# Optimization experiments

Measured on AMD Instinct MI355X. Metric: run time of the kernel, lower is better.

The kernel has to match this reference:

```python
import jax, jax.numpy as jnp
import numpy as np

N = 4096
CIN = 128
COUT = 128
J = 2
SLOPE = 0.2        # LeakyReLU negative slope (GAT-style)
NEG = -9.0e15      # mask fill value from the source
ATT = J * COUT     # att_slice


def _leaky(v):
    return jnp.where(v >= 0, v, SLOPE * v)


def setup_inputs() -> dict:
    key = jax.random.key(0)
    ks = jax.random.split(key, 12)
    x = jax.random.normal(ks[0], (N, CIN), dtype=jnp.float32)

    def sparse_op(k):
        kv, km = jax.random.split(k)
        vals = jax.random.normal(kv, (N, N), dtype=jnp.float32)
        mask = jax.random.uniform(km, (N, N)) < 0.05
        return jnp.where(mask, vals, 0.0)

    Lu = sparse_op(ks[1])
    Ld = sparse_op(ks[2])
    P = jax.random.normal(ks[3], (N, N), dtype=jnp.float32) * 0.01  # harmonic projector

    s = 1.0 / np.sqrt(CIN)
    Wi_w = jax.random.uniform(ks[4], (J, CIN, COUT), minval=-s, maxval=s)
    Wi_b = jax.random.uniform(ks[5], (J, COUT), minval=-s, maxval=s)
    Ws_w = jax.random.uniform(ks[6], (J, CIN, COUT), minval=-s, maxval=s)
    Ws_b = jax.random.uniform(ks[7], (J, COUT), minval=-s, maxval=s)
    Wh_w = jax.random.uniform(ks[8], (CIN, COUT), minval=-s, maxval=s)
    Wh_b = jax.random.uniform(ks[9], (COUT,), minval=-s, maxval=s)
    att_irr = jax.random.normal(ks[10], (2 * ATT, 1), dtype=jnp.float32) * 0.1
    att_sol = jax.random.normal(ks[11], (2 * ATT, 1), dtype=jnp.float32) * 0.1
    return {"x": x, "Lu": Lu, "Ld": Ld, "P": P,
            "Wi_w": Wi_w, "Wi_b": Wi_b, "Ws_w": Ws_w, "Ws_b": Ws_b,
            "Wh_w": Wh_w, "Wh_b": Wh_b, "att_irr": att_irr, "att_sol": att_sol}


def reference(x, Lu, Ld, P, Wi_w, Wi_b, Ws_w, Ws_b, Wh_w, Wh_b, att_irr, att_sol):
    n = x.shape[0]
    # concat_j W_irr[j](x) -> [N, J*COUT] (j-major matches torch.cat along dim=1)
    x_irr = (jnp.einsum('nc,jco->njo', x, Wi_w) + Wi_b[None]).reshape(n, ATT)
    x_sol = (jnp.einsum('nc,jco->njo', x, Ws_w) + Ws_b[None]).reshape(n, ATT)

    # GAT-style scores: E[i,j] = leaky(s1[i] + s2[j])
    E_irr = _leaky(x_irr @ att_irr[:ATT] + (x_irr @ att_irr[ATT:]).T)
    E_sol = _leaky(x_sol @ att_sol[:ATT] + (x_sol @ att_sol[ATT:]).T)
    E_irr = jnp.where(Ld != 0, E_irr, NEG)
    E_sol = jnp.where(Lu != 0, E_sol, NEG)
    alpha_irr = jax.nn.softmax(E_irr, axis=1)  # dropout: eval mode -> identity
    alpha_sol = jax.nn.softmax(E_sol, axis=1)

    z = (alpha_irr @ x) @ Wi_w[0] + Wi_b[0] + (alpha_sol @ x) @ Ws_w[0] + Ws_b[0]
    for p in range(1, J):  # Laplacian-power aggregation
        alpha_irr = alpha_irr @ Ld
        alpha_sol = alpha_sol @ Lu
        z = z + (alpha_irr @ x) @ Wi_w[p] + Wi_b[p]
        z = z + (alpha_sol @ x) @ Ws_w[p] + Ws_b[p]
    z = z + (P @ x) @ Wh_w + Wh_b
    return z
```

## Files before the change

kernel.cpp:

```cpp
#include <hip/hip_runtime.h>

#define NN 4096
#define IDX_CAP 512
#define SLOPE 0.2f

typedef float f4_t __attribute__((ext_vector_type(4)));
typedef __bf16 bf8v __attribute__((ext_vector_type(8)));
typedef float f32x16 __attribute__((ext_vector_type(16)));

#define V_OFF     0
#define C_OFF     512
#define BT_OFF    516
#define S_OFF     1024
#define HXI_OFF   32768
#define HXS_OFF   (HXI_OFF + NN*128)
#define UI_OFF    (HXS_OFF + NN*128)
#define US_OFF    (UI_OFF + NN*128)
#define XWH_OFF   (US_OFF + NN*128)
#define OI_OFF    (XWH_OFF + NN*128)
#define OS_OFF    (OI_OFF + NN*128)
#define ZP_OFF    (OS_OFF + NN*128)
#define WS_FLOATS (ZP_OFF + 8*NN*128)
#define IDX_BYTE_OFF ((size_t)WS_FLOATS * 4)
#define CNT_BYTE_OFF (IDX_BYTE_OFF + (size_t)2*NN*IDX_CAP*2)

#define XI(c)   ((c) + (((c) >> 5) << 2))

#define BMAP_BR(bid)    (((bid) >> 2) & 1)
#define BMAP_RBLK(bid)  ((((bid) >> 3) << 2) | ((bid) & 3))

#define FRAG(c, k) ((size_t)((k) >> 4) * 2048 + (size_t)((c) >> 5) * 512 \
                    + (size_t)((((c) & 31) + 32 * (((k) >> 3) & 1)) * 8 + ((k) & 7)))

__device__ __forceinline__ unsigned short f2bf(float x) {
  unsigned u = __float_as_uint(x);
  return (unsigned short)((u + 0x7FFFu + ((u >> 16) & 1u)) >> 16);
}
__device__ __forceinline__ float bf2f(unsigned short h) {
  return __uint_as_float(((unsigned)h) << 16);
}
union BFU { unsigned short u[8]; bf8v v; };

__global__ __launch_bounds__(128) void k_prep(
    const float* __restrict__ Wi_w, const float* __restrict__ Wi_b,
    const float* __restrict__ Ws_w, const float* __restrict__ Ws_b,
    const float* __restrict__ Wh_b, const float* __restrict__ att_irr,
    const float* __restrict__ att_sol, float* __restrict__ ws) {
  const int t = threadIdx.x;
  float v1i = 0.f, v2i = 0.f, v1s = 0.f, v2s = 0.f;
  for (int j = 0; j < 2; ++j) {
    for (int o = 0; o < 128; ++o) {
      const float wi = Wi_w[j*16384 + t*128 + o];
      const float wv = Ws_w[j*16384 + t*128 + o];
      v1i += wi * att_irr[j*128 + o];
      v2i += wi * att_irr[256 + j*128 + o];
      v1s += wv * att_sol[j*128 + o];
      v2s += wv * att_sol[256 + j*128 + o];
    }
  }
  ws[V_OFF + t]       = v1i;
  ws[V_OFF + 128 + t] = v2i;
  ws[V_OFF + 256 + t] = v1s;
  ws[V_OFF + 384 + t] = v2s;
  ws[BT_OFF + t] = Wi_b[t] + Wi_b[128 + t] + Ws_b[t] + Ws_b[128 + t] + Wh_b[t];
  if (t < 4) {
    const float* bb = (t < 2) ? Wi_b : Ws_b;
    const float* aa = ((t < 2) ? att_irr : att_sol) + ((t & 1) ? 256 : 0);
    float c = 0.f;
    for (int k = 0; k < 256; ++k) c += bb[k] * aa[k];
    ws[C_OFF + t] = c;
  }
}

__global__ __launch_bounds__(256) void k_pre2(
    const float* __restrict__ x, const float* __restrict__ Wh_w,
    float* __restrict__ ws, unsigned short* __restrict__ xth,
    unsigned short* __restrict__ xtl) {
  __shared__ __align__(16) float At[32][33];
  __shared__ __align__(16) float Wt[32][144];
  const int t = threadIdx.x;

  if (blockIdx.x < 128) {
    const int rb = blockIdx.x;
    const int rg = t >> 4, cg = t & 15;
    const int r0 = rb * 32;
    float acc[2][8];
    #pragma unroll
    for (int i = 0; i < 2; ++i)
      #pragma unroll
      for (int j = 0; j < 8; ++j) acc[i][j] = 0.f;
    for (int k0 = 0; k0 < 128; k0 += 32) {
      __syncthreads();
      {
        const int row = t >> 3, kq = t & 7;
        const float4 av = *(const float4*)&x[(r0 + row)*128 + k0 + kq*4];
        At[row][kq*4+0] = av.x; At[row][kq*4+1] = av.y;
        At[row][kq*4+2] = av.z; At[row][kq*4+3] = av.w;
      }
      #pragma unroll
      for (int l = 0; l < 4; ++l) {
        const int idx = t + l*256;
        const int kr = idx >> 5, c4 = idx & 31;
        const float4 wv = *(const float4*)&Wh_w[(k0 + kr)*128 + c4*4];
        *(float4*)&Wt[kr][XI(c4*4)] = wv;
      }
      __syncthreads();
      #pragma unroll
      for (int k = 0; k < 32; ++k) {
        const float a0 = At[rg*2 + 0][k];
        const float a1 = At[rg*2 + 1][k];
        const float4 b0 = *(const float4*)&Wt[k][XI(cg*8)];
        const float4 b1 = *(const float4*)&Wt[k][XI(cg*8 + 4)];
        acc[0][0] += a0*b0.x; acc[0][1] += a0*b0.y; acc[0][2] += a0*b0.z; acc[0][3] += a0*b0.w;
        acc[0][4] += a0*b1.x; acc[0][5] += a0*b1.y; acc[0][6] += a0*b1.z; acc[0][7] += a0*b1.w;
        acc[1][0] += a1*b0.x; acc[1][1] += a1*b0.y; acc[1][2] += a1*b0.z; acc[1][3] += a1*b0.w;
        acc[1][4] += a1*b1.x; acc[1][5] += a1*b1.y; acc[1][6] += a1*b1.z; acc[1][7] += a1*b1.w;
      }
    }
    #pragma unroll
    for (int i = 0; i < 2; ++i) {
      const int r = r0 + rg*2 + i;
      #pragma unroll
      for (int j = 0; j < 8; ++j) {
        const int c = cg*8 + j;
        const float val = acc[i][j];
        const unsigned short h = f2bf(val);
        const unsigned short l = f2bf(val - bf2f(h));
        const size_t fa = FRAG(c, r);
        xth[fa] = h;
        xtl[fa] = l;
      }
    }
  } else {
    const int wave = t >> 6, lane = t & 63;
    const int row = (blockIdx.x - 128) * 4 + wave;
    const float* v = ws + V_OFF;
    const float x0 = x[row*128 + lane];
    const float x1 = x[row*128 + 64 + lane];
    float p0 = x0 * v[lane]       + x1 * v[64 + lane];
    float p1 = x0 * v[128 + lane] + x1 * v[192 + lane];
    float p2 = x0 * v[256 + lane] + x1 * v[320 + lane];
    float p3 = x0 * v[384 + lane] + x1 * v[448 + lane];
    #pragma unroll
    for (int off = 32; off; off >>= 1) {
      p0 += __shfl_down(p0, off);
      p1 += __shfl_down(p1, off);
      p2 += __shfl_down(p2, off);
      p3 += __shfl_down(p3, off);
    }
    if (lane == 0) {
      ws[S_OFF + row]          = p0 + ws[C_OFF + 0];
      ws[S_OFF + NN + row]     = p1 + ws[C_OFF + 1];
      ws[S_OFF + 2*NN + row]   = p2 + ws[C_OFF + 2];
      ws[S_OFF + 3*NN + row]   = p3 + ws[C_OFF + 3];
    }
  }
}

__global__ __launch_bounds__(256) void k_spmm_emit(
    const float* __restrict__ Ld, const float* __restrict__ Lu,
    const float* __restrict__ x, float* __restrict__ ws,
    unsigned short* __restrict__ idxbuf, int* __restrict__ cntbuf) {
  const int bid = blockIdx.x;
  const int br  = BMAP_BR(bid);
  const int w = threadIdx.x >> 6, lane = threadIdx.x & 63;
  const int row = BMAP_RBLK(bid) * 4 + w;
  const float* __restrict__ Lrow = (br ? Lu : Ld) + (size_t)row * NN;
  float* __restrict__ Hx = ws + (br ? HXS_OFF : HXI_OFF);
  unsigned short* __restrict__ idxg = idxbuf + (size_t)(br*NN + row) * IDX_CAP;
  const unsigned long long lmask = (1ull << lane) - 1ull;

  __shared__ short jl[4][IDX_CAP];
  __shared__ float vl[4][IDX_CAP];

  const f4_t* __restrict__ Lrow4 = (const f4_t*)Lrow;
  int base = 0;
  #pragma unroll
  for (int c = 0; c < 4; ++c) {
    f4_t lv[4];
    #pragma unroll
    for (int i = 0; i < 4; ++i)
      lv[i] = __builtin_nontemporal_load(&Lrow4[c*256 + i*64 + lane]);
    #pragma unroll
    for (int i = 0; i < 4; ++i) {
      #pragma unroll
      for (int cc = 0; cc < 4; ++cc) {
        const float v = lv[i][cc];
        const unsigned long long bm = __ballot(v != 0.f);
        if (v != 0.f) {
          const int pos = base + (int)__popcll(bm & lmask);
          if (pos < IDX_CAP) {
            jl[w][pos] = (short)((c*256 + i*64 + lane)*4 + cc);
            vl[w][pos] = v;
          }
        }
        base += (int)__popcll(bm);
      }
    }
  }
  const int m = base;
  if (lane == 0) cntbuf[br*NN + row] = m;

  if (m <= IDX_CAP) {
    for (int p = lane; p < m; p += 64) idxg[p] = (unsigned short)jl[w][p];

    const f4_t* __restrict__ x4 = (const f4_t*)x;
    const int li = lane & 31, half = lane >> 5;
    f4_t acc = {0.f, 0.f, 0.f, 0.f};
    int p = 0;
    for (; 2*(p + 3) + 1 < m; p += 4) {
      int jj[4]; float vv[4];
      #pragma unroll
      for (int u = 0; u < 4; ++u) {
        const int q = 2*(p + u) + half;
        jj[u] = jl[w][q]; vv[u] = vl[w][q];
      }
      f4_t gg[4];
      #pragma unroll
      for (int u = 0; u < 4; ++u) gg[u] = x4[jj[u]*32 + li];
      #pragma unroll
      for (int u = 0; u < 4; ++u) acc += vv[u] * gg[u];
    }
    for (; 2*p < m; ++p) {
      const int q = 2*p + half;
      if (q < m) acc += vl[w][q] * x4[jl[w][q]*32 + li];
    }
    #pragma unroll
    for (int c = 0; c < 4; ++c) acc[c] += __shfl_xor(acc[c], 32);
    if (half == 0) *(f4_t*)&Hx[row*128 + li*4] = acc;
  } else {
    const float2* __restrict__ x2 = (const float2*)x;
    float acc0 = 0.f, acc1 = 0.f;
    for (int j = 0; j < NN; ++j) {
      const float v = Lrow[j];
      if (v != 0.f) {
        const float2 g = x2[j*64 + lane];
        acc0 += v*g.x; acc1 += v*g.y;
      }
    }
    Hx[row*128 + lane*2]     = acc0;
    Hx[row*128 + lane*2 + 1] = acc1;
  }
}

__global__ __launch_bounds__(256) void k_ugemm(
    const float* __restrict__ x, const float* __restrict__ Wi_w,
    const float* __restrict__ Ws_w, float* __restrict__ ws) {
  const int rb = blockIdx.x;
  const int sel = blockIdx.y;
  const float* A[2]; const float* W[2]; float* out;
  if (sel == 0) { A[0]=x; W[0]=Wi_w; A[1]=ws+HXI_OFF; W[1]=Wi_w+16384; out=ws+UI_OFF; }
  else          { A[0]=x; W[0]=Ws_w; A[1]=ws+HXS_OFF; W[1]=Ws_w+16384; out=ws+US_OFF; }

  __shared__ __align__(16) float At[32][33];
  __shared__ __align__(16) float Wt[32][144];
  const int t = threadIdx.x;
  const int rg = t >> 4, cg = t & 15;
  const int r0 = rb * 32;
  float acc[2][8];
  #pragma unroll
  for (int i = 0; i < 2; ++i)
    #pragma unroll
    for (int j = 0; j < 8; ++j) acc[i][j] = 0.f;

  for (int ps = 0; ps < 2; ++ps) {
    const float* __restrict__ Ap = A[ps];
    const float* __restrict__ Wp = W[ps];
    for (int k0 = 0; k0 < 128; k0 += 32) {
      __syncthreads();
      {
        const int row = t >> 3, kq = t & 7;
        const float4 av = *(const float4*)&Ap[(r0 + row)*128 + k0 + kq*4];
        At[row][kq*4+0] = av.x; At[row][kq*4+1] = av.y;
        At[row][kq*4+2] = av.z; At[row][kq*4+3] = av.w;
      }
      #pragma unroll
      for (int l = 0; l < 4; ++l) {
        const int idx = t + l*256;
        const int kr = idx >> 5, c4 = idx & 31;
        const float4 wv = *(const float4*)&Wp[(k0 + kr)*128 + c4*4];
        *(float4*)&Wt[kr][XI(c4*4)] = wv;
      }
      __syncthreads();
      #pragma unroll
      for (int k = 0; k < 32; ++k) {
        const float a0 = At[rg*2 + 0][k];
        const float a1 = At[rg*2 + 1][k];
        const float4 b0 = *(const float4*)&Wt[k][XI(cg*8)];
        const float4 b1 = *(const float4*)&Wt[k][XI(cg*8 + 4)];
        acc[0][0] += a0*b0.x; acc[0][1] += a0*b0.y; acc[0][2] += a0*b0.z; acc[0][3] += a0*b0.w;
        acc[0][4] += a0*b1.x; acc[0][5] += a0*b1.y; acc[0][6] += a0*b1.z; acc[0][7] += a0*b1.w;
        acc[1][0] += a1*b0.x; acc[1][1] += a1*b0.y; acc[1][2] += a1*b0.z; acc[1][3] += a1*b0.w;
        acc[1][4] += a1*b1.x; acc[1][5] += a1*b1.y; acc[1][6] += a1*b1.z; acc[1][7] += a1*b1.w;
      }
    }
  }
  #pragma unroll
  for (int i = 0; i < 2; ++i) {
    const int r = r0 + rg*2 + i;
    #pragma unroll
    for (int j = 0; j < 8; ++j) out[r*128 + cg*8 + j] = acc[i][j];
  }
}

__global__ __launch_bounds__(256) void k_attn(
    const float* __restrict__ Ld, const float* __restrict__ Lu,
    float* __restrict__ ws, const unsigned short* __restrict__ idxbuf,
    const int* __restrict__ cntbuf) {
  const int bid = blockIdx.x;
  const int br  = BMAP_BR(bid);
  const int w = threadIdx.x >> 6, lane = threadIdx.x & 63;
  const int row = BMAP_RBLK(bid) * 4 + w;
  const float* __restrict__ U = ws + (br ? US_OFF : UI_OFF);
  float* __restrict__ O = ws + (br ? OS_OFF : OI_OFF);
  const float s1 = ws[S_OFF + (br ? 2*NN : 0) + row];
  const float* __restrict__ s2a = ws + S_OFF + (br ? 3*NN : NN);
  const int cnt = cntbuf[br*NN + row];

  __shared__ short jl[4][IDX_CAP];
  __shared__ float el[4][IDX_CAP];

  if (cnt > 0 && cnt <= IDX_CAP) {
    const unsigned short* __restrict__ idx = idxbuf + (size_t)(br*NN + row) * IDX_CAP;
    float dpart = 0.f;
    for (int p = lane; p < cnt; p += 64) {
      const int j = idx[p];
      const float sc = s1 + s2a[j];
      const float e = expf(sc >= 0.f ? sc : SLOPE * sc);
      jl[w][p] = (short)j; el[w][p] = e; dpart += e;
    }
    #pragma unroll
    for (int off = 32; off; off >>= 1) dpart += __shfl_xor(dpart, off);
    const float rden = 1.f / dpart;

    const f4_t* __restrict__ U4 = (const f4_t*)U;
    const int li = lane & 31, half = lane >> 5;
    f4_t acc = {0.f, 0.f, 0.f, 0.f};
    int p = 0;
    for (; 2*(p + 3) + 1 < cnt; p += 4) {
      int jj[4]; float ee[4];
      #pragma unroll
      for (int u = 0; u < 4; ++u) {
        const int q = 2*(p + u) + half;
        jj[u] = jl[w][q]; ee[u] = el[w][q];
      }
      f4_t gg[4];
      #pragma unroll
      for (int u = 0; u < 4; ++u) gg[u] = U4[jj[u]*32 + li];
      #pragma unroll
      for (int u = 0; u < 4; ++u) acc += ee[u] * gg[u];
    }
    for (; 2*p < cnt; ++p) {
      const int q = 2*p + half;
      if (q < cnt) acc += el[w][q] * U4[jl[w][q]*32 + li];
    }
    #pragma unroll
    for (int c = 0; c < 4; ++c) acc[c] += __shfl_xor(acc[c], 32);
    if (half == 0) {
      acc *= rden;
      *(f4_t*)&O[row*128 + li*4] = acc;
    }
  } else if (cnt == 0) {
    const float2* __restrict__ U2 = (const float2*)U;
    float acc0 = 0.f, acc1 = 0.f;
    for (int j = 0; j < NN; ++j) {
      const float2 g = U2[j*64 + lane];
      acc0 += g.x; acc1 += g.y;
    }
    O[row*128 + lane*2]     = acc0 * (1.f / NN);
    O[row*128 + lane*2 + 1] = acc1 * (1.f / NN);
  } else {
    const float* __restrict__ Lrow = (br ? Lu : Ld) + (size_t)row * NN;
    const float2* __restrict__ U2 = (const float2*)U;
    float acc0 = 0.f, acc1 = 0.f, dp = 0.f;
    for (int j = 0; j < NN; ++j) {
      const float v = Lrow[j];
      if (v != 0.f) {
        const float sc = s1 + s2a[j];
        const float e = expf(sc >= 0.f ? sc : SLOPE * sc);
        const float2 g = U2[j*64 + lane];
        acc0 += e*g.x; acc1 += e*g.y;
        dp += e;
      }
    }
    O[row*128 + lane*2]     = acc0 / dp;
    O[row*128 + lane*2 + 1] = acc1 / dp;
  }
}

__global__ __launch_bounds__(256) void k_pgemm(
    const float* __restrict__ P, const unsigned short* __restrict__ xth,
    const unsigned short* __restrict__ xtl, float* __restrict__ zpart) {
  const int t = threadIdx.x;
  const int w = t >> 6, lane = t & 63;
  const int la = lane & 31;
  const int koff = (lane >> 5) * 8;
  const int r0 = blockIdx.x * 32;
  const int kz = blockIdx.y;
  const int kb = kz * 512 + w * 128;

  f32x16 acc[4];
  #pragma unroll
  for (int n = 0; n < 4; ++n)
    #pragma unroll
    for (int e = 0; e < 16; ++e) acc[n][e] = 0.f;

  const float* __restrict__ arow = P + (size_t)(r0 + la) * NN + kb + koff;
  const unsigned short* __restrict__ bh_base = xth + (size_t)kb * 128 + lane * 8;
  const unsigned short* __restrict__ bl_base = xtl + (size_t)kb * 128 + lane * 8;

  f4_t a0 = __builtin_nontemporal_load((const f4_t*)arow);
  f4_t a1 = __builtin_nontemporal_load((const f4_t*)(arow + 4));
  for (int s = 0; s < 8; ++s) {
    f4_t na0 = a0, na1 = a1;
    if (s < 7) {
      na0 = __builtin_nontemporal_load((const f4_t*)(arow + (s + 1) * 16));
      na1 = __builtin_nontemporal_load((const f4_t*)(arow + (s + 1) * 16 + 4));
    }
    BFU ah, al;
    #pragma unroll
    for (int i = 0; i < 8; ++i) {
      const float f = (i < 4) ? a0[i] : a1[i - 4];
      const unsigned short h = f2bf(f);
      ah.u[i] = h;
      al.u[i] = f2bf(f - bf2f(h));
    }
    const unsigned short* __restrict__ bh_s = bh_base + s * 2048;
    const unsigned short* __restrict__ bl_s = bl_base + s * 2048;
    #pragma unroll
    for (int n = 0; n < 4; ++n) {
      const bf8v bh = *(const bf8v*)(bh_s + n * 512);
      const bf8v bl = *(const bf8v*)(bl_s + n * 512);
      acc[n] = __builtin_amdgcn_mfma_f32_32x32x16_bf16(ah.v, bh, acc[n], 0, 0, 0);
      acc[n] = __builtin_amdgcn_mfma_f32_32x32x16_bf16(al.v, bh, acc[n], 0, 0, 0);
      acc[n] = __builtin_amdgcn_mfma_f32_32x32x16_bf16(ah.v, bl, acc[n], 0, 0, 0);
    }
    a0 = na0; a1 = na1;
  }

  __shared__ float red[2][32][128];
  if (w < 2) {
    #pragma unroll
    for (int n = 0; n < 4; ++n)
      #pragma unroll
      for (int reg = 0; reg < 16; ++reg) {
        const int row = (reg & 3) + 8*(reg >> 2) + 4*(lane >> 5);
        red[w][row][32*n + la] = acc[n][reg];
      }
  }
  __syncthreads();
  if (w >= 2) {
    #pragma unroll
    for (int n = 0; n < 4; ++n)
      #pragma unroll
      for (int reg = 0; reg < 16; ++reg) {
        const int row = (reg & 3) + 8*(reg >> 2) + 4*(lane >> 5);
        red[w - 2][row][32*n + la] += acc[n][reg];
      }
  }
  __syncthreads();
  float* __restrict__ zp = zpart + (size_t)kz * NN * 128;
  #pragma unroll
  for (int i = 0; i < 8; ++i) {
    const int row = w * 8 + i;
    zp[(size_t)(r0 + row) * 128 + lane]      = red[0][row][lane]      + red[1][row][lane];
    zp[(size_t)(r0 + row) * 128 + 64 + lane] = red[0][row][64 + lane] + red[1][row][64 + lane];
  }
}

__global__ __launch_bounds__(256) void k_combine(const float* __restrict__ ws,
                                                 float* __restrict__ z) {
  const int i = blockIdx.x * 256 + threadIdx.x;
  const int col = i & 127;
  float acc = ws[BT_OFF + col] + ws[OI_OFF + i] + ws[OS_OFF + i];
  #pragma unroll
  for (int kz = 0; kz < 8; ++kz) acc += ws[ZP_OFF + kz*NN*128 + i];
  z[i] = acc;
}

extern "C" void kernel_launch(void* const* d_in, const int* in_sizes, int n_in,
                              void* d_out, int out_size, void* d_ws, size_t ws_size,
                              hipStream_t stream) {
  const float* x       = (const float*)d_in[0];
  const float* Lu      = (const float*)d_in[1];
  const float* Ld      = (const float*)d_in[2];
  const float* P       = (const float*)d_in[3];
  const float* Wi_w    = (const float*)d_in[4];
  const float* Wi_b    = (const float*)d_in[5];
  const float* Ws_w    = (const float*)d_in[6];
  const float* Ws_b    = (const float*)d_in[7];
  const float* Wh_w    = (const float*)d_in[8];
  const float* Wh_b    = (const float*)d_in[9];
  const float* att_irr = (const float*)d_in[10];
  const float* att_sol = (const float*)d_in[11];
  float* z  = (float*)d_out;
  float* ws = (float*)d_ws;
  unsigned short* idxbuf = (unsigned short*)((char*)d_ws + IDX_BYTE_OFF);
  int*            cntbuf = (int*)((char*)d_ws + CNT_BYTE_OFF);
  float*          zpart  = ws + ZP_OFF;
  unsigned short* xth    = (unsigned short*)(ws + XWH_OFF);
  unsigned short* xtl    = xth + (size_t)128 * NN;

  k_prep<<<1, 128, 0, stream>>>(Wi_w, Wi_b, Ws_w, Ws_b, Wh_b, att_irr, att_sol, ws);
  k_pre2<<<1152, 256, 0, stream>>>(x, Wh_w, ws, xth, xtl);
  k_spmm_emit<<<2 * NN / 4, 256, 0, stream>>>(Ld, Lu, x, ws, idxbuf, cntbuf);
  {
    dim3 g(128, 2);
    k_ugemm<<<g, 256, 0, stream>>>(x, Wi_w, Ws_w, ws);
  }
  k_attn<<<2 * NN / 4, 256, 0, stream>>>(Ld, Lu, ws, idxbuf, cntbuf);
  {
    dim3 g(128, 8);
    k_pgemm<<<g, 256, 0, stream>>>(P, xth, xtl, zpart);
  }
  k_combine<<<NN * 128 / 256, 256, 0, stream>>>(ws, z);
}
```

Baseline: 354.7 us.

## Replace sparse gather SpMM and attention with dense split-bf16 MFMA GEMMs

The per-row nonzero compaction plus gather-based SpMM for L·x, and the index-based attention aggregation, are replaced by dense MFMA GEMMs over the full 4096-wide rows. Values are split into hi and lo bf16 parts and combined with three MFMAs to keep near-fp32 accuracy. The attention kernel computes masked exp scores inline and reduces the denominator across the 8 waves. This drops the index buffers and the divergent gathers, but does dense work on 5%-sparse matrices and launches only 256 blocks. The softmax max-subtraction is still omitted, and the empty-row fallback is gone, so a row with no nonzeros now divides by zero.

Result: slower. 444.3 us (+25.3%).

```diff
diff --git a/kernel.cpp b/kernel.cpp
--- a/kernel.cpp
+++ b/kernel.cpp
@@ -22,7 +22,6 @@
 #define ZP_OFF    (OS_OFF + NN*128)
 #define WS_FLOATS (ZP_OFF + 8*NN*128)
 #define IDX_BYTE_OFF ((size_t)WS_FLOATS * 4)
-#define CNT_BYTE_OFF (IDX_BYTE_OFF + (size_t)2*NN*IDX_CAP*2)
 
 #define XI(c)   ((c) + (((c) >> 5) << 2))
 
@@ -75,7 +74,8 @@
 __global__ __launch_bounds__(256) void k_pre2(
     const float* __restrict__ x, const float* __restrict__ Wh_w,
     float* __restrict__ ws, unsigned short* __restrict__ xth,
-    unsigned short* __restrict__ xtl) {
+    unsigned short* __restrict__ xtl, unsigned short* __restrict__ xfh,
+    unsigned short* __restrict__ xfl) {
   __shared__ __align__(16) float At[32][33];
   __shared__ __align__(16) float Wt[32][144];
   const int t = threadIdx.x;
@@ -137,6 +137,16 @@
     const float* v = ws + V_OFF;
     const float x0 = x[row*128 + lane];
     const float x1 = x[row*128 + 64 + lane];
+    {
+      const unsigned short h0 = f2bf(x0);
+      const unsigned short l0 = f2bf(x0 - bf2f(h0));
+      const size_t fa0 = FRAG(lane, row);
+      xfh[fa0] = h0; xfl[fa0] = l0;
+      const unsigned short h1 = f2bf(x1);
+      const unsigned short l1 = f2bf(x1 - bf2f(h1));
+      const size_t fa1 = FRAG(lane + 64, row);
+      xfh[fa1] = h1; xfl[fa1] = l1;
+    }
     float p0 = x0 * v[lane]       + x1 * v[64 + lane];
     float p1 = x0 * v[128 + lane] + x1 * v[192 + lane];
     float p2 = x0 * v[256 + lane] + x1 * v[320 + lane];
@@ -157,100 +167,105 @@
   }
 }
 
-__global__ __launch_bounds__(256) void k_spmm_emit(
+__global__ __launch_bounds__(512) void k_hxmm(
     const float* __restrict__ Ld, const float* __restrict__ Lu,
-    const float* __restrict__ x, float* __restrict__ ws,
-    unsigned short* __restrict__ idxbuf, int* __restrict__ cntbuf) {
+    const unsigned short* __restrict__ xfh, const unsigned short* __restrict__ xfl,
+    float* __restrict__ ws) {
   const int bid = blockIdx.x;
   const int br  = BMAP_BR(bid);
-  const int w = threadIdx.x >> 6, lane = threadIdx.x & 63;
-  const int row = BMAP_RBLK(bid) * 4 + w;
-  const float* __restrict__ Lrow = (br ? Lu : Ld) + (size_t)row * NN;
+  const int rblk = BMAP_RBLK(bid);
+  const int t = threadIdx.x;
+  const int w = t >> 6, lane = t & 63;
+  const int la = lane & 31;
+  const int koff = (lane >> 5) * 8;
+  const int r0 = rblk * 32;
+  const int kb = w * 512;
+  const float* __restrict__ L = br ? Lu : Ld;
   float* __restrict__ Hx = ws + (br ? HXS_OFF : HXI_OFF);
-  unsigned short* __restrict__ idxg = idxbuf + (size_t)(br*NN + row) * IDX_CAP;
-  const unsigned long long lmask = (1ull << lane) - 1ull;
-
-  __shared__ short jl[4][IDX_CAP];
-  __shared__ float vl[4][IDX_CAP];
-
-  const f4_t* __restrict__ Lrow4 = (const f4_t*)Lrow;
-  int base = 0;
-  #pragma unroll
-  for (int c = 0; c < 4; ++c) {
-    f4_t lv[4];
-    #pragma unroll
-    for (int i = 0; i < 4; ++i)
-      lv[i] = __builtin_nontemporal_load(&Lrow4[c*256 + i*64 + lane]);
-    #pragma unroll
-    for (int i = 0; i < 4; ++i) {
-      #pragma unroll
-      for (int cc = 0; cc < 4; ++cc) {
-        const float v = lv[i][cc];
-        const unsigned long long bm = __ballot(v != 0.f);
-        if (v != 0.f) {
-          const int pos = base + (int)__popcll(bm & lmask);
-          if (pos < IDX_CAP) {
-            jl[w][pos] = (short)((c*256 + i*64 + lane)*4 + cc);
-            vl[w][pos] = v;
-          }
-        }
-        base += (int)__popcll(bm);
-      }
-    }
-  }
-  const int m = base;
-  if (lane == 0) cntbuf[br*NN + row] = m;
-
-  if (m <= IDX_CAP) {
-    for (int p = lane; p < m; p += 64) idxg[p] = (unsigned short)jl[w][p];
-
-    const f4_t* __restrict__ x4 = (const f4_t*)x;
-    const int li = lane & 31, half = lane >> 5;
-    f4_t acc = {0.f, 0.f, 0.f, 0.f};
-    int p = 0;
-    for (; 2*(p + 3) + 1 < m; p += 4) {
-      int jj[4]; float vv[4];
-      #pragma unroll
-      for (int u = 0; u < 4; ++u) {
-        const int q = 2*(p + u) + half;
-        jj[u] = jl[w][q]; vv[u] = vl[w][q];
-      }
-      f4_t gg[4];
-      #pragma unroll
-      for (int u = 0; u < 4; ++u) gg[u] = x4[jj[u]*32 + li];
-      #pragma unroll
-      for (int u = 0; u < 4; ++u) acc += vv[u] * gg[u];
-    }
-    for (; 2*p < m; ++p) {
-      const int q = 2*p + half;
-      if (q < m) acc += vl[w][q] * x4[jl[w][q]*32 + li];
-    }
-    #pragma unroll
-    for (int c = 0; c < 4; ++c) acc[c] += __shfl_xor(acc[c], 32);
-    if (half == 0) *(f4_t*)&Hx[row*128 + li*4] = acc;
-  } else {
-    const float2* __restrict__ x2 = (const float2*)x;
-    float acc0 = 0.f, acc1 = 0.f;
-    for (int j = 0; j < NN; ++j) {
-      const float v = Lrow[j];
-      if (v != 0.f) {
-        const float2 g = x2[j*64 + lane];
-        acc0 += v*g.x; acc1 += v*g.y;
-      }
-    }
-    Hx[row*128 + lane*2]     = acc0;
-    Hx[row*128 + lane*2 + 1] = acc1;
+
+  f32x16 acc[4];
+  #pragma unroll
+  for (int n = 0; n < 4; ++n)
+    #pragma unroll
+    for (int e = 0; e < 16; ++e) acc[n][e] = 0.f;
+
+  const float* __restrict__ arow = L + (size_t)(r0 + la) * NN + kb + koff;
+  const unsigned short* __restrict__ bh_base = xfh + (size_t)kb * 128 + lane * 8;
+  const unsigned short* __restrict__ bl_base = xfl + (size_t)kb * 128 + lane * 8;
+
+  f4_t a0 = __builtin_nontemporal_load((const f4_t*)arow);
+  f4_t a1 = __builtin_nontemporal_load((const f4_t*)(arow + 4));
+  for (int s = 0; s < 32; ++s) {
+    f4_t na0 = a0, na1 = a1;
+    if (s < 31) {
+      na0 = __builtin_nontemporal_load((const f4_t*)(arow + (s + 1) * 16));
+      na1 = __builtin_nontemporal_load((const f4_t*)(arow + (s + 1) * 16 + 4));
+    }
+    BFU ah, al;
+    #pragma unroll
+    for (int i = 0; i < 8; ++i) {
+      const float f = (i < 4) ? a0[i] : a1[i - 4];
+      const unsigned short h = f2bf(f);
+      ah.u[i] = h;
+      al.u[i] = f2bf(f - bf2f(h));
+    }
+    const unsigned short* __restrict__ bh_s = bh_base + s * 2048;
+    const unsigned short* __restrict__ bl_s = bl_base + s * 2048;
+    #pragma unroll
+    for (int n = 0; n < 4; ++n) {
+      const bf8v bh = *(const bf8v*)(bh_s + n * 512);
+      const bf8v bl = *(const bf8v*)(bl_s + n * 512);
+      acc[n] = __builtin_amdgcn_mfma_f32_32x32x16_bf16(ah.v, bh, acc[n], 0, 0, 0);
+      acc[n] = __builtin_amdgcn_mfma_f32_32x32x16_bf16(al.v, bh, acc[n], 0, 0, 0);
+      acc[n] = __builtin_amdgcn_mfma_f32_32x32x16_bf16(ah.v, bl, acc[n], 0, 0, 0);
+    }
+    a0 = na0; a1 = na1;
+  }
+
+  __shared__ float red[4][32][128];
+  if (w < 4) {
+    #pragma unroll
+    for (int n = 0; n < 4; ++n)
+      #pragma unroll
+      for (int reg = 0; reg < 16; ++reg) {
+        const int row = (reg & 3) + 8*(reg >> 2) + 4*(lane >> 5);
+        red[w][row][32*n + la] = acc[n][reg];
+      }
+  }
+  __syncthreads();
+  if (w >= 4) {
+    #pragma unroll
+    for (int n = 0; n < 4; ++n)
+      #pragma unroll
+      for (int reg = 0; reg < 16; ++reg) {
+        const int row = (reg & 3) + 8*(reg >> 2) + 4*(lane >> 5);
+        red[w - 4][row][32*n + la] += acc[n][reg];
+      }
+  }
+  __syncthreads();
+  {
+    const int row = t >> 4;
+    const int c0 = (t & 15) * 8;
+    #pragma unroll
+    for (int j = 0; j < 8; ++j) {
+      const int c = c0 + j;
+      Hx[(size_t)(r0 + row) * 128 + c] =
+          red[0][row][c] + red[1][row][c] + red[2][row][c] + red[3][row][c];
+    }
   }
 }
 
 __global__ __launch_bounds__(256) void k_ugemm(
     const float* __restrict__ x, const float* __restrict__ Wi_w,
-    const float* __restrict__ Ws_w, float* __restrict__ ws) {
+    const float* __restrict__ Ws_w, float* __restrict__ ws,
+    unsigned short* __restrict__ uih, unsigned short* __restrict__ uil,
+    unsigned short* __restrict__ ush, unsigned short* __restrict__ usl) {
   const int rb = blockIdx.x;
   const int sel = blockIdx.y;
-  const float* A[2]; const float* W[2]; float* out;
-  if (sel == 0) { A[0]=x; W[0]=Wi_w; A[1]=ws+HXI_OFF; W[1]=Wi_w+16384; out=ws+UI_OFF; }
-  else          { A[0]=x; W[0]=Ws_w; A[1]=ws+HXS_OFF; W[1]=Ws_w+16384; out=ws+US_OFF; }
+  const float* A[2]; const float* W[2];
+  unsigned short* uh; unsigned short* ul;
+  if (sel == 0) { A[0]=x; W[0]=Wi_w; A[1]=ws+HXI_OFF; W[1]=Wi_w+16384; uh=uih; ul=uil; }
+  else          { A[0]=x; W[0]=Ws_w; A[1]=ws+HXS_OFF; W[1]=Ws_w+16384; uh=ush; ul=usl; }
 
   __shared__ __align__(16) float At[32][33];
   __shared__ __align__(16) float Wt[32][144];
@@ -299,92 +314,121 @@
   for (int i = 0; i < 2; ++i) {
     const int r = r0 + rg*2 + i;
     #pragma unroll
-    for (int j = 0; j < 8; ++j) out[r*128 + cg*8 + j] = acc[i][j];
-  }
-}
-
-__global__ __launch_bounds__(256) void k_attn(
+    for (int j = 0; j < 8; ++j) {
+      const int c = cg*8 + j;
+      const float val = acc[i][j];
+      const unsigned short h = f2bf(val);
+      const unsigned short l = f2bf(val - bf2f(h));
+      const size_t fa = FRAG(c, r);
+      uh[fa] = h;
+      ul[fa] = l;
+    }
+  }
+}
+
+__global__ __launch_bounds__(512) void k_attnmm(
     const float* __restrict__ Ld, const float* __restrict__ Lu,
-    float* __restrict__ ws, const unsigned short* __restrict__ idxbuf,
-    const int* __restrict__ cntbuf) {
+    float* __restrict__ ws, const unsigned short* __restrict__ uih,
+    const unsigned short* __restrict__ uil, const unsigned short* __restrict__ ush,
+    const unsigned short* __restrict__ usl) {
   const int bid = blockIdx.x;
   const int br  = BMAP_BR(bid);
-  const int w = threadIdx.x >> 6, lane = threadIdx.x & 63;
-  const int row = BMAP_RBLK(bid) * 4 + w;
-  const float* __restrict__ U = ws + (br ? US_OFF : UI_OFF);
+  const int rblk = BMAP_RBLK(bid);
+  const int t = threadIdx.x;
+  const int w = t >> 6, lane = t & 63;
+  const int la = lane & 31;
+  const int koff = (lane >> 5) * 8;
+  const int r0 = rblk * 32;
+  const int kb = w * 512;
+  const float* __restrict__ L = br ? Lu : Ld;
+  const unsigned short* __restrict__ ufh = br ? ush : uih;
+  const unsigned short* __restrict__ ufl = br ? usl : uil;
   float* __restrict__ O = ws + (br ? OS_OFF : OI_OFF);
-  const float s1 = ws[S_OFF + (br ? 2*NN : 0) + row];
-  const float* __restrict__ s2a = ws + S_OFF + (br ? 3*NN : NN);
-  const int cnt = cntbuf[br*NN + row];
-
-  __shared__ short jl[4][IDX_CAP];
-  __shared__ float el[4][IDX_CAP];
-
-  if (cnt > 0 && cnt <= IDX_CAP) {
-    const unsigned short* __restrict__ idx = idxbuf + (size_t)(br*NN + row) * IDX_CAP;
-    float dpart = 0.f;
-    for (int p = lane; p < cnt; p += 64) {
-      const int j = idx[p];
-      const float sc = s1 + s2a[j];
-      const float e = expf(sc >= 0.f ? sc : SLOPE * sc);
-      jl[w][p] = (short)j; el[w][p] = e; dpart += e;
-    }
-    #pragma unroll
-    for (int off = 32; off; off >>= 1) dpart += __shfl_xor(dpart, off);
-    const float rden = 1.f / dpart;
-
-    const f4_t* __restrict__ U4 = (const f4_t*)U;
-    const int li = lane & 31, half = lane >> 5;
-    f4_t acc = {0.f, 0.f, 0.f, 0.f};
-    int p = 0;
-    for (; 2*(p + 3) + 1 < cnt; p += 4) {
-      int jj[4]; float ee[4];
-      #pragma unroll
-      for (int u = 0; u < 4; ++u) {
-        const int q = 2*(p + u) + half;
-        jj[u] = jl[w][q]; ee[u] = el[w][q];
-      }
-      f4_t gg[4];
-      #pragma unroll
-      for (int u = 0; u < 4; ++u) gg[u] = U4[jj[u]*32 + li];
-      #pragma unroll
-      for (int u = 0; u < 4; ++u) acc += ee[u] * gg[u];
-    }
-    for (; 2*p < cnt; ++p) {
-      const int q = 2*p + half;
-      if (q < cnt) acc += el[w][q] * U4[jl[w][q]*32 + li];
-    }
-    #pragma unroll
-    for (int c = 0; c < 4; ++c) acc[c] += __shfl_xor(acc[c], 32);
-    if (half == 0) {
-      acc *= rden;
-      *(f4_t*)&O[row*128 + li*4] = acc;
-    }
-  } else if (cnt == 0) {
-    const float2* __restrict__ U2 = (const float2*)U;
-    float acc0 = 0.f, acc1 = 0.f;
-    for (int j = 0; j < NN; ++j) {
-      const float2 g = U2[j*64 + lane];
-      acc0 += g.x; acc1 += g.y;
-    }
-    O[row*128 + lane*2]     = acc0 * (1.f / NN);
-    O[row*128 + lane*2 + 1] = acc1 * (1.f / NN);
-  } else {
-    const float* __restrict__ Lrow = (br ? Lu : Ld) + (size_t)row * NN;
-    const float2* __restrict__ U2 = (const float2*)U;
-    float acc0 = 0.f, acc1 = 0.f, dp = 0.f;
-    for (int j = 0; j < NN; ++j) {
-      const float v = Lrow[j];
-      if (v != 0.f) {
-        const float sc = s1 + s2a[j];
-        const float e = expf(sc >= 0.f ? sc : SLOPE * sc);
-        const float2 g = U2[j*64 + lane];
-        acc0 += e*g.x; acc1 += e*g.y;
-        dp += e;
-      }
-    }
-    O[row*128 + lane*2]     = acc0 / dp;
-    O[row*128 + lane*2 + 1] = acc1 / dp;
+  const float s1v = ws[S_OFF + (br ? 2*NN : 0) + r0 + la];
+  const float* __restrict__ s2p = ws + S_OFF + (br ? 3*NN : NN) + kb + koff;
+
+  f32x16 acc[4];
+  #pragma unroll
+  for (int n = 0; n < 4; ++n)
+    #pragma unroll
+    for (int e = 0; e < 16; ++e) acc[n][e] = 0.f;
+  float dp = 0.f;
+
+  const float* __restrict__ arow = L + (size_t)(r0 + la) * NN + kb + koff;
+  const unsigned short* __restrict__ bh_base = ufh + (size_t)kb * 128 + lane * 8;
+  const unsigned short* __restrict__ bl_base = ufl + (size_t)kb * 128 + lane * 8;
+
+  f4_t a0 = __builtin_nontemporal_load((const f4_t*)arow);
+  f4_t a1 = __builtin_nontemporal_load((const f4_t*)(arow + 4));
+  for (int s = 0; s < 32; ++s) {
+    f4_t na0 = a0, na1 = a1;
+    if (s < 31) {
+      na0 = __builtin_nontemporal_load((const f4_t*)(arow + (s + 1) * 16));
+      na1 = __builtin_nontemporal_load((const f4_t*)(arow + (s + 1) * 16 + 4));
+    }
+    const f4_t s2a = *(const f4_t*)(s2p + s * 16);
+    const f4_t s2b = *(const f4_t*)(s2p + s * 16 + 4);
+    BFU eh, el;
+    #pragma unroll
+    for (int i = 0; i < 8; ++i) {
+      const float Lv = (i < 4) ? a0[i] : a1[i - 4];
+      const float s2 = (i < 4) ? s2a[i] : s2b[i - 4];
+      const float sc = s1v + s2;
+      const float ex = (Lv != 0.f) ? expf(sc >= 0.f ? sc : SLOPE * sc) : 0.f;
+      dp += ex;
+      const unsigned short h = f2bf(ex);
+      eh.u[i] = h;
+      el.u[i] = f2bf(ex - bf2f(h));
+    }
+    const unsigned short* __restrict__ bh_s = bh_base + s * 2048;
+    const unsigned short* __restrict__ bl_s = bl_base + s * 2048;
+    #pragma unroll
+    for (int n = 0; n < 4; ++n) {
+      const bf8v bh = *(const bf8v*)(bh_s + n * 512);
+      const bf8v bl = *(const bf8v*)(bl_s + n * 512);
+      acc[n] = __builtin_amdgcn_mfma_f32_32x32x16_bf16(eh.v, bh, acc[n], 0, 0, 0);
+      acc[n] = __builtin_amdgcn_mfma_f32_32x32x16_bf16(el.v, bh, acc[n], 0, 0, 0);
+      acc[n] = __builtin_amdgcn_mfma_f32_32x32x16_bf16(eh.v, bl, acc[n], 0, 0, 0);
+    }
+    a0 = na0; a1 = na1;
+  }
+  dp += __shfl_xor(dp, 32);
+
+  __shared__ float red[4][32][128];
+  __shared__ float dsl[4][32];
+  if (w < 4) {
+    #pragma unroll
+    for (int n = 0; n < 4; ++n)
+      #pragma unroll
+      for (int reg = 0; reg < 16; ++reg) {
+        const int row = (reg & 3) + 8*(reg >> 2) + 4*(lane >> 5);
+        red[w][row][32*n + la] = acc[n][reg];
+      }
+    if (lane < 32) dsl[w][la] = dp;
+  }
+  __syncthreads();
+  if (w >= 4) {
+    #pragma unroll
+    for (int n = 0; n < 4; ++n)
+      #pragma unroll
+      for (int reg = 0; reg < 16; ++reg) {
+        const int row = (reg & 3) + 8*(reg >> 2) + 4*(lane >> 5);
+        red[w - 4][row][32*n + la] += acc[n][reg];
+      }
+    if (lane < 32) dsl[w - 4][la] += dp;
+  }
+  __syncthreads();
+  {
+    const int row = t >> 4;
+    const int c0 = (t & 15) * 8;
+    const float den = dsl[0][row] + dsl[1][row] + dsl[2][row] + dsl[3][row];
+    const float rden = 1.f / den;
+    #pragma unroll
+    for (int j = 0; j < 8; ++j) {
+      const int c = c0 + j;
+      O[(size_t)(r0 + row) * 128 + c] =
+          (red[0][row][c] + red[1][row][c] + red[2][row][c] + red[3][row][c]) * rden;
+    }
   }
 }
 
@@ -495,20 +539,24 @@
   const float* att_sol = (const float*)d_in[11];
   float* z  = (float*)d_out;
   float* ws = (float*)d_ws;
-  unsigned short* idxbuf = (unsigned short*)((char*)d_ws + IDX_BYTE_OFF);
-  int*            cntbuf = (int*)((char*)d_ws + CNT_BYTE_OFF);
-  float*          zpart  = ws + ZP_OFF;
-  unsigned short* xth    = (unsigned short*)(ws + XWH_OFF);
-  unsigned short* xtl    = xth + (size_t)128 * NN;
+  float*          zpart = ws + ZP_OFF;
+  unsigned short* xth   = (unsigned short*)(ws + XWH_OFF);
+  unsigned short* xtl   = xth + (size_t)128 * NN;
+  unsigned short* uih   = (unsigned short*)(ws + UI_OFF);
+  unsigned short* uil   = uih + (size_t)128 * NN;
+  unsigned short* ush   = (unsigned short*)(ws + US_OFF);
+  unsigned short* usl   = ush + (size_t)128 * NN;
+  unsigned short* xfh   = (unsigned short*)((char*)d_ws + IDX_BYTE_OFF);
+  unsigned short* xfl   = xfh + (size_t)128 * NN;
 
   k_prep<<<1, 128, 0, stream>>>(Wi_w, Wi_b, Ws_w, Ws_b, Wh_b, att_irr, att_sol, ws);
-  k_pre2<<<1152, 256, 0, stream>>>(x, Wh_w, ws, xth, xtl);
-  k_spmm_emit<<<2 * NN / 4, 256, 0, stream>>>(Ld, Lu, x, ws, idxbuf, cntbuf);
+  k_pre2<<<1152, 256, 0, stream>>>(x, Wh_w, ws, xth, xtl, xfh, xfl);
+  k_hxmm<<<256, 512, 0, stream>>>(Ld, Lu, xfh, xfl, ws);
   {
     dim3 g(128, 2);
-    k_ugemm<<<g, 256, 0, stream>>>(x, Wi_w, Ws_w, ws);
-  }
-  k_attn<<<2 * NN / 4, 256, 0, stream>>>(Ld, Lu, ws, idxbuf, cntbuf);
+    k_ugemm<<<g, 256, 0, stream>>>(x, Wi_w, Ws_w, ws, uih, uil, ush, usl);
+  }
+  k_attnmm<<<256, 512, 0, stream>>>(Ld, Lu, ws, uih, uil, ush, usl);
   {
     dim3 g(128, 8);
     k_pgemm<<<g, 256, 0, stream>>>(P, xth, xtl, zpart);
```
